# Kernel tuning notes

Measured on AMD Instinct MI355X. Metric: run time of the kernel, lower is better.

Reference implementation:

```python
import jax, jax.numpy as jnp
import numpy as np

B, T, C, H, E, K = 4, 2048, 512, 2048, 8, 2


def setup_inputs() -> dict:
    key = jax.random.key(0)
    ks = jax.random.split(key, 7)
    s_r = 1.0 / np.sqrt(C)
    s_h = 1.0 / np.sqrt(H)
    return {
        "x": jax.random.normal(ks[0], (B, T, C), dtype=jnp.float32),
        "Wr": jax.random.uniform(ks[1], (C, E), jnp.float32, -s_r, s_r),
        "br": jax.random.uniform(ks[2], (E,), jnp.float32, -s_r, s_r),
        "W1": jax.random.uniform(ks[3], (E, C, H), jnp.float32, -s_r, s_r),
        "b1": jax.random.uniform(ks[4], (E, H), jnp.float32, -s_r, s_r),
        "W2": jax.random.uniform(ks[5], (E, H, C), jnp.float32, -s_h, s_h),
        "b2": jax.random.uniform(ks[6], (E, C), jnp.float32, -s_h, s_h),
    }


def reference(x, Wr, br, W1, b1, W2, b2):
    # Router logits [B,T,E]
    logits = jnp.einsum("btc,ce->bte", x, Wr) + br
    topk_vals, topk_idx = jax.lax.top_k(logits, K)  # [B,T,K]
    scores = jax.nn.softmax(topk_vals, axis=-1)  # softmax over the K selected
    # Combine weights per expert: gate[b,t,e] = sum_k scores[b,t,k]*(idx==e)
    onehot = jax.nn.one_hot(topk_idx, E, dtype=x.dtype)  # [B,T,K,E]
    gate = jnp.einsum("btk,btke->bte", scores, onehot)  # [B,T,E]
    # Dense-masked expert MLPs (tokens not routed to e have gate==0)
    h = jax.nn.relu(jnp.einsum("btc,ech->bteh", x, W1) + b1)  # [B,T,E,H]
    y = jnp.einsum("bteh,ehc->btec", h, W2) + b2  # [B,T,E,C]
    out = jnp.einsum("btec,bte->btc", y, gate)  # weighted combine
    return logits, topk_idx, out
```

## Files before the change

### kernel.cpp

```cpp
#include <hip/hip_runtime.h>
#include <hip/hip_bf16.h>

#define NTOK 8192
#define NASN 16384
#define C_ 512
#define H_ 2048
#define E_ 8
#define RBC 2048

typedef __bf16 bf16x8 __attribute__((ext_vector_type(8)));
typedef float f32x4 __attribute__((ext_vector_type(4)));

#define WS_COUNTS 0
#define WS_OFFS   65536
#define WS_T1S    65792
#define WS_INFO   66048
#define WS_TOKL   (WS_INFO + NTOK*16)
#define WS_SLOTS  (WS_TOKL + NASN*4)
#define WS_XBF    (WS_SLOTS + NTOK*8)
#define WS_W1B    (WS_XBF + (size_t)NTOK*C_*2)
#define WS_W2B    (WS_W1B + (size_t)E_*H_*C_*2)
#define WS_HS     (WS_W2B + (size_t)E_*H_*C_*2)
#define WS_YS     WS_XBF

__device__ __forceinline__ unsigned int f2bf(float f) {
  __hip_bfloat16 h = __float2bfloat16(f);
  return (unsigned int)*(unsigned short*)&h;
}
__device__ __forceinline__ float bf2f(unsigned int u) {
  return __int_as_float((u & 0xffffu) << 16);
}

__device__ __forceinline__ void g2l16(const unsigned short* g, unsigned short* l) {
  __builtin_amdgcn_global_load_lds(
      (const __attribute__((address_space(1))) unsigned int*)g,
      (__attribute__((address_space(3))) unsigned int*)l, 16, 0, 0);
}

__device__ __forceinline__ void stage_decode(int L, int& brow, int& q) {
  int s = L >> 3, slot = L & 7;
  int v = slot ^ (s & 7);
  brow = 2*s + (v >> 2);
  q = v & 3;
}

__global__ __launch_bounds__(256) void k_fused(
    const float* __restrict__ x, const float* __restrict__ Wr,
    const float* __restrict__ br, float* __restrict__ out_logits,
    float* __restrict__ out_idx, int4* __restrict__ info,
    int* __restrict__ counts, unsigned short* __restrict__ Xbf,
    const float* __restrict__ W1, unsigned short* __restrict__ W1b,
    const float* __restrict__ W2, unsigned short* __restrict__ W2b)
{
  __shared__ float tileS[128][33];
  __shared__ int bc[8];
  int b = blockIdx.x;
  int tid = threadIdx.x;

  if (b < RBC) {
    if (tid < 8) bc[tid] = 0;
    __syncthreads();
    int t = b * 4 + (tid >> 6);
    int lane = tid & 63;
    const float4* xr = (const float4*)(x + (size_t)t * C_);
    float4 x0 = xr[lane*2], x1 = xr[lane*2+1];
    uint4 pk;
    pk.x = f2bf(x0.x) | (f2bf(x0.y) << 16);
    pk.y = f2bf(x0.z) | (f2bf(x0.w) << 16);
    pk.z = f2bf(x1.x) | (f2bf(x1.y) << 16);
    pk.w = f2bf(x1.z) | (f2bf(x1.w) << 16);
    *(uint4*)(Xbf + (size_t)t * C_ + lane*8) = pk;

    float xs[8] = {x0.x,x0.y,x0.z,x0.w,x1.x,x1.y,x1.z,x1.w};
    float acc[8] = {0,0,0,0,0,0,0,0};
    #pragma unroll
    for (int j = 0; j < 8; j++) {
      const float4* w = (const float4*)(Wr + (size_t)(lane*8+j) * E_);
      float4 w0 = w[0], w1 = w[1];
      float we[8] = {w0.x,w0.y,w0.z,w0.w,w1.x,w1.y,w1.z,w1.w};
      #pragma unroll
      for (int e = 0; e < 8; e++) acc[e] += xs[j] * we[e];
    }
    #pragma unroll
    for (int off = 1; off < 64; off <<= 1) {
      #pragma unroll
      for (int e = 0; e < 8; e++) acc[e] += __shfl_xor(acc[e], off, 64);
    }
    #pragma unroll
    for (int e = 0; e < 8; e++) acc[e] += br[e];
    if (lane == 0) {
      #pragma unroll
      for (int e = 0; e < 8; e++) out_logits[t*8 + e] = acc[e];
      int i0 = 0; float v0 = acc[0];
      #pragma unroll
      for (int e = 1; e < 8; e++) if (acc[e] > v0) { v0 = acc[e]; i0 = e; }
      int i1 = -1; float v1 = -1e30f;
      #pragma unroll
      for (int e = 0; e < 8; e++) if (e != i0 && acc[e] > v1) { v1 = acc[e]; i1 = e; }
      float d = expf(v1 - v0);
      float s1 = d / (1.0f + d);
      float s0 = 1.0f - s1;
      out_idx[t*2]     = (float)i0;
      out_idx[t*2 + 1] = (float)i1;
      info[t] = make_int4(i0, i1, __float_as_int(s0), __float_as_int(s1));
      atomicAdd(&bc[i0], 1);
      atomicAdd(&bc[i1], 1);
    }
    __syncthreads();
    if (tid < 8) counts[b*8 + tid] = bc[tid];
    return;
  }

  const float* in; unsigned short* outp; int R, S, bx, by, bz;
  if (b < 2*RBC) {
    int bb = b - RBC;
    in = W1; outp = W1b; R = C_; S = H_;
    bx = bb & 63; by = (bb >> 6) & 3; bz = bb >> 8;
  } else {
    int bb = b - 2*RBC;
    in = W2; outp = W2b; R = H_; S = C_;
    bx = bb & 15; by = (bb >> 4) & 15; bz = bb >> 8;
  }
  size_t zo = (size_t)bz * R * S;
  in += zo; outp += zo;
  int r0 = by * 128, s0 = bx * 32;
  #pragma unroll
  for (int i = 0; i < 4; i++) {
    int lin = i*256 + tid;
    int rr = lin >> 3, sq = lin & 7;
    float4 v = *(const float4*)(in + (size_t)(r0 + rr) * S + s0 + sq*4);
    tileS[rr][sq*4+0] = v.x;
    tileS[rr][sq*4+1] = v.y;
    tileS[rr][sq*4+2] = v.z;
    tileS[rr][sq*4+3] = v.w;
  }
  __syncthreads();
  #pragma unroll
  for (int i = 0; i < 4; i++) {
    int lin = i*256 + tid;
    int ss = lin >> 5, rq = lin & 31;
    ushort4 v;
    v.x = (unsigned short)f2bf(tileS[rq*4+0][ss]);
    v.y = (unsigned short)f2bf(tileS[rq*4+1][ss]);
    v.z = (unsigned short)f2bf(tileS[rq*4+2][ss]);
    v.w = (unsigned short)f2bf(tileS[rq*4+3][ss]);
    *(ushort4*)(outp + (size_t)(s0 + ss) * R + r0 + rq*4) = v;
  }
}

__global__ __launch_bounds__(256) void k_prefscatter(
    const int* __restrict__ counts, const int4* __restrict__ info,
    int* __restrict__ tokl, int2* __restrict__ slots2,
    int* __restrict__ offs, int* __restrict__ t1s)
{
  __shared__ int full_s[8][32];
  __shared__ int part_s[8][32];
  __shared__ int tot_s[8];
  __shared__ int off_s[9];
  __shared__ int cur[8];
  int c = blockIdx.x, t = threadIdx.x;
  int e = t & 7, g = t >> 3;
  int lim = c * 16;
  int full = 0, part = 0;
  for (int i = 0; i < 64; i++) {
    int rb = g*64 + i;
    int v = counts[rb*8 + e];
    full += v;
    if (rb < lim) part += v;
  }
  full_s[e][g] = full; part_s[e][g] = part;
  __syncthreads();
  if (t < 8) {
    int s = 0;
    #pragma unroll
    for (int gg = 0; gg < 32; gg++) s += full_s[t][gg];
    tot_s[t] = s;
  }
  __syncthreads();
  if (t == 0) {
    int o = 0;
    off_s[0] = 0;
    for (int ee = 0; ee < 8; ee++) { o += tot_s[ee]; off_s[ee+1] = o; }
    if (c == 0) {
      offs[0] = 0; t1s[0] = 0;
      int tt = 0;
      for (int ee = 0; ee < 8; ee++) {
        offs[ee+1] = off_s[ee+1];
        tt += (tot_s[ee] + 127) >> 7;
        t1s[ee+1] = tt;
      }
    }
  }
  __syncthreads();
  if (t < 8) {
    int mg = c >> 2;
    int bse = off_s[t];
    #pragma unroll
    for (int gg = 0; gg < 32; gg++) if (gg < mg) bse += full_s[t][gg];
    bse += part_s[t][mg];
    cur[t] = bse;
  }
  __syncthreads();
  if (t < 64) {
    int tok = c*64 + t;
    int4 nfo = info[tok];
    int r0 = atomicAdd(&cur[nfo.x], 1);
    int r1 = atomicAdd(&cur[nfo.y], 1);
    tokl[r0] = tok;
    tokl[r1] = tok;
    slots2[tok] = make_int2(r0, r1);
  }
}

#define KLOOP(KI)                                                              \
  {                                                                            \
    int cOff = 0, sOff = 2*8192;                                               \
    for (int ki = 0; ki < (KI); ki++) {                                        \
      if (ki + 1 < (KI))                                                       \
        asm volatile("s_waitcnt vmcnt(2)" ::: "memory");                       \
      else                                                                     \
        asm volatile("s_waitcnt vmcnt(0)" ::: "memory");                       \
      asm volatile("s_barrier" ::: "memory");                                  \
      if (ki + 2 < (KI)) {                                                     \
        int off_ = (ki + 2) * 32;                                              \
        unsigned short* nb_ = AB + sOff;                                       \
        g2l16(ga + off_, nb_ + lao);                                           \
        g2l16(gb + off_, nb_ + lbo);                                           \
      }                                                                        \
      const unsigned short* Ap_ = AB + cOff;                                   \
      const unsigned short* Bp_ = Ap_ + 4096;                                  \
      bf16x8 af0 = *(const bf16x8*)&Ap_[wm*32 + 0*512 + rbase];                \
      bf16x8 af1 = *(const bf16x8*)&Ap_[wm*32 + 1*512 + rbase];                \
      bf16x8 bf0 = *(const bf16x8*)&Bp_[wn*32 + 0*512 + rbase];                \
      bf16x8 bf1 = *(const bf16x8*)&Bp_[wn*32 + 1*512 + rbase];                \
      __builtin_amdgcn_s_setprio(1);                                           \
      acc[0][0] = __builtin_amdgcn_mfma_f32_16x16x32_bf16(af0, bf0, acc[0][0], 0, 0, 0); \
      acc[0][1] = __builtin_amdgcn_mfma_f32_16x16x32_bf16(af0, bf1, acc[0][1], 0, 0, 0); \
      acc[1][0] = __builtin_amdgcn_mfma_f32_16x16x32_bf16(af1, bf0, acc[1][0], 0, 0, 0); \
      acc[1][1] = __builtin_amdgcn_mfma_f32_16x16x32_bf16(af1, bf1, acc[1][1], 0, 0, 0); \
      __builtin_amdgcn_s_setprio(0);                                           \
      bf16x8 af2 = *(const bf16x8*)&Ap_[wm*32 + 2*512 + rbase];                \
      bf16x8 af3 = *(const bf16x8*)&Ap_[wm*32 + 3*512 + rbase];                \
      __builtin_amdgcn_s_setprio(1);                                           \
      acc[2][0] = __builtin_amdgcn_mfma_f32_16x16x32_bf16(af2, bf0, acc[2][0], 0, 0, 0); \
      acc[2][1] = __builtin_amdgcn_mfma_f32_16x16x32_bf16(af2, bf1, acc[2][1], 0, 0, 0); \
      acc[3][0] = __builtin_amdgcn_mfma_f32_16x16x32_bf16(af3, bf0, acc[3][0], 0, 0, 0); \
      acc[3][1] = __builtin_amdgcn_mfma_f32_16x16x32_bf16(af3, bf1, acc[3][1], 0, 0, 0); \
      __builtin_amdgcn_s_setprio(0);                                           \
      asm volatile("s_waitcnt lgkmcnt(0)" ::: "memory");                       \
      cOff += 8192; if (cOff == 3*8192) cOff = 0;                              \
      sOff += 8192; if (sOff == 3*8192) sOff = 0;                              \
    }                                                                          \
  }

__global__ __launch_bounds__(512) void k_gemm1(
    const unsigned short* __restrict__ Xbf, const int* __restrict__ tokl,
    const unsigned short* __restrict__ W1b,
    const float* __restrict__ b1, unsigned short* __restrict__ Hs,
    const int* __restrict__ offs, const int* __restrict__ t1s)
{
  __shared__ __align__(16) unsigned short AB[3*8192];
  int b = blockIdx.x;
  int mo = b >> 7, rr = b & 127;
  int n0 = (rr >> 3) * 128;
  int mt = mo*8 + (rr & 7);
  if (mt >= t1s[8]) return;
  int e = 0;
  #pragma unroll
  for (int i = 0; i < 7; i++) if (mt >= t1s[e+1]) e++;
  int row0 = offs[e] + (mt - t1s[e]) * 128;
  int rowEnd = offs[e+1];
  int tid = threadIdx.x, lane = tid & 63, w = tid >> 6;
  int wm = (w >> 2) * 64, wn = (w & 3) * 32;
  int quad = lane >> 4, l16 = lane & 15;
  const f32x4 zero = {0.f, 0.f, 0.f, 0.f};
  f32x4 acc[4][2];
  #pragma unroll
  for (int i = 0; i < 4; i++)
    #pragma unroll
    for (int j = 0; j < 2; j++) acc[i][j] = zero;
  const unsigned short* Bsrc = W1b + ((size_t)e * H_ + n0) * C_;

  const unsigned short* ga; const unsigned short* gb;
  int lao, lbo;
  {
    int L = w*64 + lane;
    int brow, q; stage_decode(L, brow, q);
    int gr = row0 + brow; gr = gr < NASN-1 ? gr : NASN-1;
    int trow = tokl[gr];
    ga = Xbf + (size_t)trow * C_ + q*8;
    gb = Bsrc + (size_t)brow * C_ + q*8;
    lao = w*512;
    lbo = 4096 + w*512;
  }
  int rbase = (l16>>1)*64 + ((((l16&1)<<2) + quad) ^ (l16>>1))*8;
  const int KI = C_ / 32;

  g2l16(ga, AB + lao);            g2l16(gb, AB + lbo);
  g2l16(ga + 32, AB + 8192 + lao); g2l16(gb + 32, AB + 8192 + lbo);

  KLOOP(KI);
  __syncthreads();

  unsigned short* Lt = AB + w*2048;
  #pragma unroll
  for (int j = 0; j < 2; j++) {
    int n = n0 + wn + j*16 + l16;
    float bias = b1[e * H_ + n];
    #pragma unroll
    for (int i = 0; i < 4; i++)
      #pragma unroll
      for (int r = 0; r < 4; r++) {
        float v = acc[i][j][r] + bias;
        Lt[(i*16 + quad*4 + r)*32 + j*16 + l16] = (unsigned short)f2bf(v > 0.f ? v : 0.f);
      }
  }
  #pragma unroll
  for (int it = 0; it < 4; it++) {
    int rloc = it*16 + (lane >> 2);
    int m = row0 + wm + rloc;
    uint4 vv = *(uint4*)&Lt[rloc*32 + (lane & 3)*8];
    if (m < rowEnd)
      *(uint4*)(Hs + (size_t)m * H_ + n0 + wn + (lane & 3)*8) = vv;
  }
}

__global__ __launch_bounds__(512) void k_gemm2(
    const unsigned short* __restrict__ Hs, const unsigned short* __restrict__ W2b,
    const float* __restrict__ b2, unsigned short* __restrict__ Ys,
    const int* __restrict__ offs, const int* __restrict__ t1s)
{
  __shared__ __align__(16) unsigned short AB[3*8192];
  int b = blockIdx.x;
  int mo = b >> 5, rr = b & 31;
  int n0 = (rr >> 3) * 128;
  int mt = mo*8 + (rr & 7);
  if (mt >= t1s[8]) return;
  int e = 0;
  #pragma unroll
  for (int i = 0; i < 7; i++) if (mt >= t1s[e+1]) e++;
  int row0 = offs[e] + (mt - t1s[e]) * 128;
  int rowEnd = offs[e+1];
  int tid = threadIdx.x, lane = tid & 63, w = tid >> 6;
  int wm = (w >> 2) * 64, wn = (w & 3) * 32;
  int quad = lane >> 4, l16 = lane & 15;
  const f32x4 zero = {0.f, 0.f, 0.f, 0.f};
  f32x4 acc[4][2];
  #pragma unroll
  for (int i = 0; i < 4; i++)
    #pragma unroll
    for (int j = 0; j < 2; j++) acc[i][j] = zero;
  const unsigned short* Bsrc = W2b + ((size_t)e * C_ + n0) * H_;

  const unsigned short* ga; const unsigned short* gb;
  int lao, lbo;
  {
    int L = w*64 + lane;
    int brow, q; stage_decode(L, brow, q);
    int gr = row0 + brow; gr = gr < NASN-1 ? gr : NASN-1;
    ga = Hs + (size_t)gr * H_ + q*8;
    gb = Bsrc + (size_t)brow * H_ + q*8;
    lao = w*512;
    lbo = 4096 + w*512;
  }
  int rbase = (l16>>1)*64 + ((((l16&1)<<2) + quad) ^ (l16>>1))*8;
  const int KI = H_ / 32;

  g2l16(ga, AB + lao);            g2l16(gb, AB + lbo);
  g2l16(ga + 32, AB + 8192 + lao); g2l16(gb + 32, AB + 8192 + lbo);

  KLOOP(KI);
  __syncthreads();

  unsigned short* Lt = AB + w*2048;
  #pragma unroll
  for (int j = 0; j < 2; j++) {
    int n = n0 + wn + j*16 + l16;
    float bias = b2[e * C_ + n];
    #pragma unroll
    for (int i = 0; i < 4; i++)
      #pragma unroll
      for (int r = 0; r < 4; r++)
        Lt[(i*16 + quad*4 + r)*32 + j*16 + l16] =
            (unsigned short)f2bf(acc[i][j][r] + bias);
  }
  #pragma unroll
  for (int it = 0; it < 4; it++) {
    int rloc = it*16 + (lane >> 2);
    int m = row0 + wm + rloc;
    uint4 vv = *(uint4*)&Lt[rloc*32 + (lane & 3)*8];
    if (m < rowEnd)
      *(uint4*)(Ys + (size_t)m * C_ + n0 + wn + (lane & 3)*8) = vv;
  }
}

__global__ __launch_bounds__(256) void k_combine(
    const unsigned short* __restrict__ Ys, const int4* __restrict__ info,
    const int2* __restrict__ slots2, float* __restrict__ outp)
{
  int t = blockIdx.x * 4 + (threadIdx.x >> 6);
  int lane = threadIdx.x & 63;
  int4 nfo = info[t];
  int2 ss = slots2[t];
  float g0 = __int_as_float(nfo.z), g1 = __int_as_float(nfo.w);
  uint4 a = *(const uint4*)(Ys + (size_t)ss.x * C_ + lane*8);
  uint4 bb = *(const uint4*)(Ys + (size_t)ss.y * C_ + lane*8);
  unsigned int au[4] = {a.x, a.y, a.z, a.w};
  unsigned int bu[4] = {bb.x, bb.y, bb.z, bb.w};
  float vals[8];
  #pragma unroll
  for (int q = 0; q < 4; q++) {
    vals[q*2]   = g0*bf2f(au[q])       + g1*bf2f(bu[q]);
    vals[q*2+1] = g0*bf2f(au[q] >> 16) + g1*bf2f(bu[q] >> 16);
  }
  float4 o0, o1;
  o0.x = vals[0]; o0.y = vals[1]; o0.z = vals[2]; o0.w = vals[3];
  o1.x = vals[4]; o1.y = vals[5]; o1.z = vals[6]; o1.w = vals[7];
  float4* o = (float4*)(outp + (size_t)t * C_ + lane*8);
  o[0] = o0;
  o[1] = o1;
}

extern "C" void kernel_launch(void* const* d_in, const int* in_sizes, int n_in,
                              void* d_out, int out_size, void* d_ws, size_t ws_size,
                              hipStream_t stream)
{
  const float* x  = (const float*)d_in[0];
  const float* Wr = (const float*)d_in[1];
  const float* br = (const float*)d_in[2];
  const float* W1 = (const float*)d_in[3];
  const float* b1 = (const float*)d_in[4];
  const float* W2 = (const float*)d_in[5];
  const float* b2 = (const float*)d_in[6];
  float* out = (float*)d_out;
  char* ws = (char*)d_ws;

  int*  counts = (int*)(ws + WS_COUNTS);
  int*  offs   = (int*)(ws + WS_OFFS);
  int*  t1s    = (int*)(ws + WS_T1S);
  int4* info   = (int4*)(ws + WS_INFO);
  int*  tokl   = (int*)(ws + WS_TOKL);
  int2* slots2 = (int2*)(ws + WS_SLOTS);
  unsigned short* Xbf = (unsigned short*)(ws + WS_XBF);
  unsigned short* W1b = (unsigned short*)(ws + WS_W1B);
  unsigned short* W2b = (unsigned short*)(ws + WS_W2B);
  unsigned short* Hs  = (unsigned short*)(ws + WS_HS);
  unsigned short* Ys  = (unsigned short*)(ws + WS_YS);

  k_fused<<<3*RBC, 256, 0, stream>>>(x, Wr, br, out, out + 65536, info,
                                     counts, Xbf, W1, W1b, W2, W2b);
  k_prefscatter<<<128, 256, 0, stream>>>(counts, info, tokl, slots2, offs, t1s);
  k_gemm1<<<17*128, 512, 0, stream>>>(Xbf, tokl, W1b, b1, Hs, offs, t1s);
  k_gemm2<<<17*32, 512, 0, stream>>>(Hs, W2b, b2, Ys, offs, t1s);
  k_combine<<<NTOK/4, 256, 0, stream>>>(Ys, info, slots2, out + 81920);
}
```

Baseline: 260.6 us.

## Widen gemm1 tile to 128x256 and move W2 bf16 transpose into gemm1 launch

The first expert GEMM now uses 128x256 output tiles, giving each wave a 64x64 sub-tile with 16 accumulators. This doubles A-tile reuse and halves the number of gathered X loads per output. The W2 fp32-to-bf16 transpose moves out of the front fused kernel into extra blocks appended to the gemm1 launch, so it can overlap with GEMM work instead of sitting on the critical path before routing. The trade-offs are more LDS and registers per block, which can lower occupancy, and transpose blocks that compete with GEMM blocks.

```diff
diff --git a/kernel.cpp b/kernel.cpp
--- a/kernel.cpp
+++ b/kernel.cpp
@@ -7,6 +7,7 @@
 #define H_ 2048
 #define E_ 8
 #define RBC 2048
+#define G1BLK 1088
 
 typedef __bf16 bf16x8 __attribute__((ext_vector_type(8)));
 typedef float f32x4 __attribute__((ext_vector_type(4)));
@@ -49,8 +50,7 @@
     const float* __restrict__ br, float* __restrict__ out_logits,
     float* __restrict__ out_idx, int4* __restrict__ info,
     int* __restrict__ counts, unsigned short* __restrict__ Xbf,
-    const float* __restrict__ W1, unsigned short* __restrict__ W1b,
-    const float* __restrict__ W2, unsigned short* __restrict__ W2b)
+    const float* __restrict__ W1, unsigned short* __restrict__ W1b)
 {
   __shared__ float tileS[128][33];
   __shared__ int bc[8];
@@ -111,16 +111,10 @@
     return;
   }
 
-  const float* in; unsigned short* outp; int R, S, bx, by, bz;
-  if (b < 2*RBC) {
-    int bb = b - RBC;
-    in = W1; outp = W1b; R = C_; S = H_;
-    bx = bb & 63; by = (bb >> 6) & 3; bz = bb >> 8;
-  } else {
-    int bb = b - 2*RBC;
-    in = W2; outp = W2b; R = H_; S = C_;
-    bx = bb & 15; by = (bb >> 4) & 15; bz = bb >> 8;
-  }
+  int bb = b - RBC;
+  const float* in = W1; unsigned short* outp = W1b;
+  int R = C_, S = H_;
+  int bx = bb & 63, by = (bb >> 6) & 3, bz = bb >> 8;
   size_t zo = (size_t)bz * R * S;
   in += zo; outp += zo;
   int r0 = by * 128, s0 = bx * 32;
@@ -209,6 +203,162 @@
     tokl[r0] = tok;
     tokl[r1] = tok;
     slots2[tok] = make_int2(r0, r1);
+  }
+}
+
+__global__ __launch_bounds__(512) void k_gemm1(
+    const unsigned short* __restrict__ Xbf, const int* __restrict__ tokl,
+    const unsigned short* __restrict__ W1b,
+    const float* __restrict__ b1, unsigned short* __restrict__ Hs,
+    const int* __restrict__ offs, const int* __restrict__ t1s,
+    const float* __restrict__ W2, unsigned short* __restrict__ W2b)
+{
+  __shared__ __align__(16) unsigned short AB[3*12288];
+  int b = blockIdx.x;
+  int tid = threadIdx.x;
+
+  if (b >= G1BLK) {
+    float* tS = (float*)AB;
+    int b2 = b - G1BLK;
+    int bx = b2 & 7, by = (b2 >> 3) & 15, bz = b2 >> 7;
+    const float* in = W2 + (size_t)bz * H_ * C_;
+    unsigned short* outp = W2b + (size_t)bz * H_ * C_;
+    int r0 = by * 128, s0 = bx * 64;
+    #pragma unroll
+    for (int i = 0; i < 4; i++) {
+      int lin = i*512 + tid;
+      int rr = lin >> 4, cq = lin & 15;
+      float4 v = *(const float4*)(in + (size_t)(r0 + rr) * C_ + s0 + cq*4);
+      tS[rr*65 + cq*4+0] = v.x;
+      tS[rr*65 + cq*4+1] = v.y;
+      tS[rr*65 + cq*4+2] = v.z;
+      tS[rr*65 + cq*4+3] = v.w;
+    }
+    __syncthreads();
+    #pragma unroll
+    for (int i = 0; i < 4; i++) {
+      int lin = i*512 + tid;
+      int ss = lin >> 5, rq = lin & 31;
+      ushort4 v;
+      v.x = (unsigned short)f2bf(tS[(rq*4+0)*65 + ss]);
+      v.y = (unsigned short)f2bf(tS[(rq*4+1)*65 + ss]);
+      v.z = (unsigned short)f2bf(tS[(rq*4+2)*65 + ss]);
+      v.w = (unsigned short)f2bf(tS[(rq*4+3)*65 + ss]);
+      *(ushort4*)(outp + (size_t)(s0 + ss) * H_ + r0 + rq*4) = v;
+    }
+    return;
+  }
+
+  int mo = b >> 6, rr = b & 63;
+  int n0 = (rr >> 3) * 256;
+  int mt = mo*8 + (rr & 7);
+  if (mt >= t1s[8]) return;
+  int e = 0;
+  #pragma unroll
+  for (int i = 0; i < 7; i++) if (mt >= t1s[i+1]) e++;
+  int row0 = offs[e] + (mt - t1s[e]) * 128;
+  int rowEnd = offs[e+1];
+  int lane = tid & 63, w = tid >> 6;
+  int wm = (w >> 2) * 64, wn = (w & 3) * 64;
+  int quad = lane >> 4, l16 = lane & 15;
+  const f32x4 zero = {0.f, 0.f, 0.f, 0.f};
+  f32x4 acc[4][4];
+  #pragma unroll
+  for (int i = 0; i < 4; i++)
+    #pragma unroll
+    for (int j = 0; j < 4; j++) acc[i][j] = zero;
+  const unsigned short* Bsrc = W1b + ((size_t)e * H_ + n0) * C_;
+
+  const unsigned short* ga; int lao;
+  const unsigned short* gb[2]; int lbo[2];
+  {
+    int L = w*64 + lane;
+    int brow, q; stage_decode(L, brow, q);
+    int gr = row0 + brow; gr = gr < NASN-1 ? gr : NASN-1;
+    int trow = tokl[gr];
+    ga = Xbf + (size_t)trow * C_ + q*8;
+    lao = w*512;
+  }
+  #pragma unroll
+  for (int j = 0; j < 2; j++) {
+    int L = (w*2 + j)*64 + lane;
+    int brow, q; stage_decode(L, brow, q);
+    gb[j] = Bsrc + (size_t)brow * C_ + q*8;
+    lbo[j] = 4096 + (w*2 + j)*512;
+  }
+  int rbase = (l16>>1)*64 + ((((l16&1)<<2) + quad) ^ (l16>>1))*8;
+  const int KI = C_ / 32;
+
+  g2l16(ga, AB + lao);
+  g2l16(gb[0], AB + lbo[0]); g2l16(gb[1], AB + lbo[1]);
+  g2l16(ga + 32, AB + 12288 + lao);
+  g2l16(gb[0] + 32, AB + 12288 + lbo[0]); g2l16(gb[1] + 32, AB + 12288 + lbo[1]);
+
+  {
+    int cOff = 0, sOff = 2*12288;
+    for (int ki = 0; ki < KI; ki++) {
+      if (ki + 1 < KI)
+        asm volatile("s_waitcnt vmcnt(3)" ::: "memory");
+      else
+        asm volatile("s_waitcnt vmcnt(0)" ::: "memory");
+      asm volatile("s_barrier" ::: "memory");
+      if (ki + 2 < KI) {
+        int off_ = (ki + 2) * 32;
+        unsigned short* nb_ = AB + sOff;
+        g2l16(ga + off_, nb_ + lao);
+        g2l16(gb[0] + off_, nb_ + lbo[0]);
+        g2l16(gb[1] + off_, nb_ + lbo[1]);
+      }
+      const unsigned short* Ap_ = AB + cOff;
+      const unsigned short* Bp_ = Ap_ + 4096;
+      bf16x8 af_[4], bf_[4];
+      #pragma unroll
+      for (int i = 0; i < 4; i++)
+        af_[i] = *(const bf16x8*)&Ap_[wm*32 + i*512 + rbase];
+      #pragma unroll
+      for (int j = 0; j < 4; j++)
+        bf_[j] = *(const bf16x8*)&Bp_[wn*32 + j*512 + rbase];
+      __builtin_amdgcn_s_setprio(1);
+      #pragma unroll
+      for (int i = 0; i < 4; i++)
+        #pragma unroll
+        for (int j = 0; j < 2; j++)
+          acc[i][j] = __builtin_amdgcn_mfma_f32_16x16x32_bf16(af_[i], bf_[j], acc[i][j], 0, 0, 0);
+      __builtin_amdgcn_s_setprio(0);
+      __builtin_amdgcn_s_setprio(1);
+      #pragma unroll
+      for (int i = 0; i < 4; i++)
+        #pragma unroll
+        for (int j = 2; j < 4; j++)
+          acc[i][j] = __builtin_amdgcn_mfma_f32_16x16x32_bf16(af_[i], bf_[j], acc[i][j], 0, 0, 0);
+      __builtin_amdgcn_s_setprio(0);
+      asm volatile("s_waitcnt lgkmcnt(0)" ::: "memory");
+      cOff += 12288; if (cOff == 3*12288) cOff = 0;
+      sOff += 12288; if (sOff == 3*12288) sOff = 0;
+    }
+  }
+  __syncthreads();
+
+  unsigned short* Lt = AB + w*4096;
+  #pragma unroll
+  for (int j = 0; j < 4; j++) {
+    int n = n0 + wn + j*16 + l16;
+    float bias = b1[e * H_ + n];
+    #pragma unroll
+    for (int i = 0; i < 4; i++)
+      #pragma unroll
+      for (int r = 0; r < 4; r++) {
+        float v = acc[i][j][r] + bias;
+        Lt[(i*16 + quad*4 + r)*64 + j*16 + l16] = (unsigned short)f2bf(v > 0.f ? v : 0.f);
+      }
+  }
+  #pragma unroll
+  for (int it = 0; it < 8; it++) {
+    int rloc = it*8 + (lane >> 3);
+    int m = row0 + wm + rloc;
+    uint4 vv = *(uint4*)&Lt[rloc*64 + (lane & 7)*8];
+    if (m < rowEnd)
+      *(uint4*)(Hs + (size_t)m * H_ + n0 + wn + (lane & 7)*8) = vv;
   }
 }
 
@@ -253,78 +403,6 @@
     }                                                                          \
   }
 
-__global__ __launch_bounds__(512) void k_gemm1(
-    const unsigned short* __restrict__ Xbf, const int* __restrict__ tokl,
-    const unsigned short* __restrict__ W1b,
-    const float* __restrict__ b1, unsigned short* __restrict__ Hs,
-    const int* __restrict__ offs, const int* __restrict__ t1s)
-{
-  __shared__ __align__(16) unsigned short AB[3*8192];
-  int b = blockIdx.x;
-  int mo = b >> 7, rr = b & 127;
-  int n0 = (rr >> 3) * 128;
-  int mt = mo*8 + (rr & 7);
-  if (mt >= t1s[8]) return;
-  int e = 0;
-  #pragma unroll
-  for (int i = 0; i < 7; i++) if (mt >= t1s[e+1]) e++;
-  int row0 = offs[e] + (mt - t1s[e]) * 128;
-  int rowEnd = offs[e+1];
-  int tid = threadIdx.x, lane = tid & 63, w = tid >> 6;
-  int wm = (w >> 2) * 64, wn = (w & 3) * 32;
-  int quad = lane >> 4, l16 = lane & 15;
-  const f32x4 zero = {0.f, 0.f, 0.f, 0.f};
-  f32x4 acc[4][2];
-  #pragma unroll
-  for (int i = 0; i < 4; i++)
-    #pragma unroll
-    for (int j = 0; j < 2; j++) acc[i][j] = zero;
-  const unsigned short* Bsrc = W1b + ((size_t)e * H_ + n0) * C_;
-
-  const unsigned short* ga; const unsigned short* gb;
-  int lao, lbo;
-  {
-    int L = w*64 + lane;
-    int brow, q; stage_decode(L, brow, q);
-    int gr = row0 + brow; gr = gr < NASN-1 ? gr : NASN-1;
-    int trow = tokl[gr];
-    ga = Xbf + (size_t)trow * C_ + q*8;
-    gb = Bsrc + (size_t)brow * C_ + q*8;
-    lao = w*512;
-    lbo = 4096 + w*512;
-  }
-  int rbase = (l16>>1)*64 + ((((l16&1)<<2) + quad) ^ (l16>>1))*8;
-  const int KI = C_ / 32;
-
-  g2l16(ga, AB + lao);            g2l16(gb, AB + lbo);
-  g2l16(ga + 32, AB + 8192 + lao); g2l16(gb + 32, AB + 8192 + lbo);
-
-  KLOOP(KI);
-  __syncthreads();
-
-  unsigned short* Lt = AB + w*2048;
-  #pragma unroll
-  for (int j = 0; j < 2; j++) {
-    int n = n0 + wn + j*16 + l16;
-    float bias = b1[e * H_ + n];
-    #pragma unroll
-    for (int i = 0; i < 4; i++)
-      #pragma unroll
-      for (int r = 0; r < 4; r++) {
-        float v = acc[i][j][r] + bias;
-        Lt[(i*16 + quad*4 + r)*32 + j*16 + l16] = (unsigned short)f2bf(v > 0.f ? v : 0.f);
-      }
-  }
-  #pragma unroll
-  for (int it = 0; it < 4; it++) {
-    int rloc = it*16 + (lane >> 2);
-    int m = row0 + wm + rloc;
-    uint4 vv = *(uint4*)&Lt[rloc*32 + (lane & 3)*8];
-    if (m < rowEnd)
-      *(uint4*)(Hs + (size_t)m * H_ + n0 + wn + (lane & 3)*8) = vv;
-  }
-}
-
 __global__ __launch_bounds__(512) void k_gemm2(
     const unsigned short* __restrict__ Hs, const unsigned short* __restrict__ W2b,
     const float* __restrict__ b2, unsigned short* __restrict__ Ys,
@@ -447,10 +525,11 @@
   unsigned short* Hs  = (unsigned short*)(ws + WS_HS);
   unsigned short* Ys  = (unsigned short*)(ws + WS_YS);
 
-  k_fused<<<3*RBC, 256, 0, stream>>>(x, Wr, br, out, out + 65536, info,
-                                     counts, Xbf, W1, W1b, W2, W2b);
+  k_fused<<<2*RBC, 256, 0, stream>>>(x, Wr, br, out, out + 65536, info,
+                                     counts, Xbf, W1, W1b);
   k_prefscatter<<<128, 256, 0, stream>>>(counts, info, tokl, slots2, offs, t1s);
-  k_gemm1<<<17*128, 512, 0, stream>>>(Xbf, tokl, W1b, b1, Hs, offs, t1s);
+  k_gemm1<<<G1BLK + 1024, 512, 0, stream>>>(Xbf, tokl, W1b, b1, Hs, offs, t1s,
+                                            W2, W2b);
   k_gemm2<<<17*32, 512, 0, stream>>>(Hs, W2b, b2, Ys, offs, t1s);
   k_combine<<<NTOK/4, 256, 0, stream>>>(Ys, info, slots2, out + 81920);
 }
```

New measurement: 257.4 us. Within noise of the previous version (-1.2%).
